# Performance work log

Hardware: AMD Instinct MI355X
Metric: run time of the kernel (lower is better)

## Reference

```python
import jax, jax.numpy as jnp
import numpy as np

B, S, D = 1, 2048, 4096
H, HK, HD = 32, 8, 128  # query heads, kv heads, head dim
T_CACHE = 2048
N_REP = H // HK


def setup_inputs() -> dict:
    key = jax.random.key(0)
    ks = jax.random.split(key, 8)
    x = jax.random.normal(ks[0], (B, S, D), dtype=jnp.float32)
    # multiplicative rope factor, broadcast over head axis
    rope = jax.random.uniform(ks[1], (1, S, 1, HD), dtype=jnp.float32, minval=-1.0, maxval=1.0)
    cache_k = jax.random.normal(ks[2], (B, T_CACHE, HK, HD), dtype=jnp.float32)
    cache_v = jax.random.normal(ks[3], (B, T_CACHE, HK, HD), dtype=jnp.float32)
    wq = jax.random.normal(ks[4], (D, H * HD), dtype=jnp.float32) * 0.02
    wk = jax.random.normal(ks[5], (D, HK * HD), dtype=jnp.float32) * 0.02
    wv = jax.random.normal(ks[6], (D, HK * HD), dtype=jnp.float32) * 0.02
    wo = jax.random.normal(ks[7], (H * HD, D), dtype=jnp.float32) * 0.02
    # mask: [1, 1, S, T_CACHE + S]; attend freely to cache, causal within new chunk
    neg = np.float32(-1e9)
    causal = np.triu(np.full((S, S), neg, dtype=np.float32), k=1)
    mask = np.concatenate([np.zeros((S, T_CACHE), dtype=np.float32), causal], axis=1)
    mask = jnp.asarray(mask)[None, None, :, :]
    return {"x": x, "rope": rope, "mask": mask, "cache_k": cache_k,
            "cache_v": cache_v, "wq": wq, "wk": wk, "wv": wv, "wo": wo}


def reference(x, rope, mask, cache_k, cache_v, wq, wk, wv, wo):
    b, s, _ = x.shape
    scale = 1.0 / np.sqrt(HD).astype(np.float32)
    xq = (x @ wq).reshape(b, s, H, HD) * rope          # [b, s, H, hd]
    xk = (x @ wk).reshape(b, s, HK, HD) * rope         # [b, s, HK, hd]
    xv = (x @ wv).reshape(b, s, HK, HD)
    keys = jnp.concatenate([cache_k, xk], axis=1)      # [b, t, HK, hd]
    vals = jnp.concatenate([cache_v, xv], axis=1)
    keys = jnp.repeat(keys, N_REP, axis=2)             # GQA repeat -> [b, t, H, hd]
    vals = jnp.repeat(vals, N_REP, axis=2)
    scores = jnp.einsum('bshd,bthd->bhst', xq, keys) * scale
    scores = scores + mask
    probs = jax.nn.softmax(scores.astype(jnp.float32), axis=-1).astype(xq.dtype)
    out = jnp.einsum('bhst,bthd->bshd', probs, vals).reshape(b, s, H * HD)
    return out @ wo
```

## Files before the change

kernel.cpp:

```cpp
#include <hip/hip_runtime.h>

typedef unsigned short u16;
typedef unsigned int   u32;
typedef short  s16x8 __attribute__((ext_vector_type(8)));
typedef float  f32x4 __attribute__((ext_vector_type(4)));

__device__ __forceinline__ u16 f2bf(float f) {
    union { float f; u32 i; } x; x.f = f;
    u32 r = x.i + 0x7FFFu + ((x.i >> 16) & 1u);
    return (u16)(r >> 16);
}

__device__ __forceinline__ void gld16(const void* g, void* l) {
    __builtin_amdgcn_global_load_lds((const __attribute__((address_space(1))) void*)g,
                                     (__attribute__((address_space(3))) void*)l,
                                     16, 0, 0);
}

__global__ __launch_bounds__(256)
void cast_bf16(const float* __restrict__ in, u16* __restrict__ out, int n4) {
    int g = blockIdx.x * 256 + threadIdx.x;
    if (g >= n4) return;
    float4 v = ((const float4*)in)[g];
    ushort4 o; o.x = f2bf(v.x); o.y = f2bf(v.y); o.z = f2bf(v.z); o.w = f2bf(v.w);
    ((ushort4*)out)[g] = o;
}

__global__ __launch_bounds__(256)
void tconv(const float* __restrict__ B, u16* __restrict__ Bt, int K, int N) {
    __shared__ float T[32][33];
    int n0 = blockIdx.x * 32, k0 = blockIdx.y * 32;
    int t = threadIdx.x;
    int r = t >> 3, c4 = (t & 7) * 4;
    float4 v = *(const float4*)&B[(size_t)(k0 + r) * N + n0 + c4];
    T[r][c4 + 0] = v.x; T[r][c4 + 1] = v.y; T[r][c4 + 2] = v.z; T[r][c4 + 3] = v.w;
    __syncthreads();
    ushort4 o;
    o.x = f2bf(T[c4 + 0][r]); o.y = f2bf(T[c4 + 1][r]);
    o.z = f2bf(T[c4 + 2][r]); o.w = f2bf(T[c4 + 3][r]);
    *(ushort4*)&Bt[(size_t)(n0 + r) * K + k0 + c4] = o;
}

__global__ __launch_bounds__(256)
void kcache_conv(const float* __restrict__ ck, u16* __restrict__ Kc) {
    int g = blockIdx.x * 256 + threadIdx.x;
    int d = (g & 31) * 4, kh = (g >> 5) & 7, t = g >> 8;
    float4 v = *(const float4*)&ck[(size_t)t * 1024 + kh * 128 + d];
    ushort4 o; o.x = f2bf(v.x); o.y = f2bf(v.y); o.z = f2bf(v.z); o.w = f2bf(v.w);
    *(ushort4*)&Kc[(size_t)kh * 524288 + (size_t)t * 128 + d] = o;
}

__global__ __launch_bounds__(256)
void vcache_conv(const float* __restrict__ cv, u16* __restrict__ Vt) {
    __shared__ float T[32][33];
    int t0 = blockIdx.x * 32, d0 = blockIdx.y * 32, kh = blockIdx.z;
    int t = threadIdx.x;
    int r = t >> 3, c4 = (t & 7) * 4;
    float4 v = *(const float4*)&cv[(size_t)(t0 + r) * 1024 + kh * 128 + d0 + c4];
    T[r][c4 + 0] = v.x; T[r][c4 + 1] = v.y; T[r][c4 + 2] = v.z; T[r][c4 + 3] = v.w;
    __syncthreads();
    ushort4 o;
    o.x = f2bf(T[c4 + 0][r]); o.y = f2bf(T[c4 + 1][r]);
    o.z = f2bf(T[c4 + 2][r]); o.w = f2bf(T[c4 + 3][r]);
    *(ushort4*)&Vt[(size_t)(kh * 128 + d0 + r) * 4096 + t0 + c4] = o;
}

__device__ __forceinline__ void gemm_core(const u16* __restrict__ A,
                                          const u16* __restrict__ Bt,
                                          int K, int m0,
                                          u16* As, u16* Bs, f32x4 acc[4][4])
{
    const int tid = threadIdx.x;
    const int lane = tid & 63, w = tid >> 6;
    const int quad = lane >> 4, l15 = lane & 15;
    const int mw = (w >> 1) * 64, nw = (w & 1) * 64;
    const int lrow = tid >> 2;
    const int lcol = ((tid & 3) ^ (lrow & 3)) * 8;
    const int rsw = l15 & 3;

    for (int k0 = 0; k0 < K; k0 += 32) {
        __syncthreads();
        gld16(A  + (size_t)(m0 +      lrow) * K + k0 + lcol, &As[w * 512]);
        gld16(A  + (size_t)(m0 + 64 + lrow) * K + k0 + lcol, &As[2048 + w * 512]);
        gld16(Bt + (size_t)(           lrow) * K + k0 + lcol, &Bs[w * 512]);
        gld16(Bt + (size_t)(      64 + lrow) * K + k0 + lcol, &Bs[2048 + w * 512]);
        __syncthreads();
        s16x8 af[4], bf[4];
        #pragma unroll
        for (int i = 0; i < 4; ++i)
            af[i] = *(const s16x8*)&As[(mw + i * 16 + l15) * 32 + (quad ^ rsw) * 8];
        #pragma unroll
        for (int j = 0; j < 4; ++j)
            bf[j] = *(const s16x8*)&Bs[(nw + j * 16 + l15) * 32 + (quad ^ rsw) * 8];
        #pragma unroll
        for (int i = 0; i < 4; ++i)
            #pragma unroll
            for (int j = 0; j < 4; ++j)
                acc[i][j] = __builtin_amdgcn_mfma_f32_16x16x32_bf16(
                    af[i], bf[j], acc[i][j], 0, 0, 0);
    }
}

__global__ __launch_bounds__(256, 2)
void gemm_qkv(const u16* __restrict__ A, const u16* __restrict__ Wq,
              const u16* __restrict__ Wk, const u16* __restrict__ Wv,
              u16* __restrict__ Qw, u16* __restrict__ Kc, u16* __restrict__ Vt,
              const float* __restrict__ rope)
{
    __shared__ u16 As[128 * 32];
    __shared__ u16 Bs[128 * 32];
    const int m0 = blockIdx.y * 128, n0 = blockIdx.x * 128;

    const u16* Bt;
    if (n0 < 4096)       Bt = Wq + (size_t)n0 * 4096;
    else if (n0 < 5120)  Bt = Wk + (size_t)(n0 - 4096) * 4096;
    else                 Bt = Wv + (size_t)(n0 - 5120) * 4096;

    f32x4 acc[4][4];
    #pragma unroll
    for (int i = 0; i < 4; ++i)
        #pragma unroll
        for (int j = 0; j < 4; ++j) acc[i][j] = (f32x4)0.f;

    gemm_core(A, Bt, 4096, m0, As, Bs, acc);

    const int lane = threadIdx.x & 63, w = threadIdx.x >> 6;
    const int quad = lane >> 4, l15 = lane & 15;
    const int mw = (w >> 1) * 64, nw = (w & 1) * 64;

    #pragma unroll
    for (int i = 0; i < 4; ++i) {
        #pragma unroll
        for (int j = 0; j < 4; ++j) {
            int mm = m0 + mw + i * 16 + quad * 4;
            int nn = n0 + nw + j * 16 + l15;
            if (nn < 4096) {
                #pragma unroll
                for (int r = 0; r < 4; ++r)
                    Qw[(size_t)(mm + r) * 4096 + nn] =
                        f2bf(acc[i][j][r] * rope[(size_t)(mm + r) * 128 + (nn & 127)]
                             * 0.08838834764831845f);
            } else if (nn < 5120) {
                #pragma unroll
                for (int r = 0; r < 4; ++r)
                    Kc[(size_t)((nn - 4096) >> 7) * 524288
                       + (size_t)(2048 + mm + r) * 128 + (nn & 127)] =
                        f2bf(acc[i][j][r] * rope[(size_t)(mm + r) * 128 + (nn & 127)]);
            } else {
                ushort4 o;
                o.x = f2bf(acc[i][j][0]); o.y = f2bf(acc[i][j][1]);
                o.z = f2bf(acc[i][j][2]); o.w = f2bf(acc[i][j][3]);
                *(ushort4*)&Vt[(size_t)(nn - 5120) * 4096 + 2048 + mm] = o;
            }
        }
    }
}

__global__ __launch_bounds__(256, 2)
void gemm_wo(const u16* __restrict__ A, const u16* __restrict__ Bt,
             float* __restrict__ C)
{
    __shared__ u16 As[128 * 32];
    __shared__ u16 Bs[128 * 32];
    const int m0 = blockIdx.y * 128, n0 = blockIdx.x * 128;

    f32x4 acc[4][4];
    #pragma unroll
    for (int i = 0; i < 4; ++i)
        #pragma unroll
        for (int j = 0; j < 4; ++j) acc[i][j] = (f32x4)0.f;

    gemm_core(A, Bt + (size_t)n0 * 4096, 4096, m0, As, Bs, acc);

    const int lane = threadIdx.x & 63, w = threadIdx.x >> 6;
    const int quad = lane >> 4, l15 = lane & 15;
    const int mw = (w >> 1) * 64, nw = (w & 1) * 64;

    #pragma unroll
    for (int i = 0; i < 4; ++i)
        #pragma unroll
        for (int j = 0; j < 4; ++j) {
            int mm = m0 + mw + i * 16 + quad * 4;
            int nn = n0 + nw + j * 16 + l15;
            #pragma unroll
            for (int r = 0; r < 4; ++r)
                C[(size_t)(mm + r) * 4096 + nn] = acc[i][j][r];
        }
}

__global__ __launch_bounds__(256, 2)
void attn_mfma(const u16* __restrict__ Qw, const u16* __restrict__ Kc,
               const u16* __restrict__ Vt, u16* __restrict__ AO)
{
    __shared__ u16 Ks[64 * 128];
    __shared__ u16 Vs[128 * 64];
    __shared__ u16 Qs[64 * 136];
    __shared__ u16 Pb[64 * 72];
    __shared__ float Ls[2][64];

    const int tid = threadIdx.x;
    const int lane = tid & 63, w = tid >> 6;
    const int quad = lane >> 4, l15 = lane & 15;
    const int h = blockIdx.x, kh = h >> 2;
    const int q0 = blockIdx.y * 64;
    const int kw = w & 1, qw = w >> 1;
    const size_t kvb = (size_t)kh * 524288;

    #pragma unroll
    for (int i = 0; i < 4; ++i) {
        int g = tid + i * 256;
        int row = g >> 4, c8 = (g & 15) * 8;
        *(s16x8*)&Qs[row * 136 + c8] =
            *(const s16x8*)&Qw[(size_t)(q0 + row) * 4096 + h * 128 + c8];
    }

    f32x4 o[2][4];
    #pragma unroll
    for (int m = 0; m < 2; ++m)
        #pragma unroll
        for (int n = 0; n < 4; ++n) o[m][n] = (f32x4)0.f;
    float lacc[2] = {0.f, 0.f};

    const int krow = tid >> 4, kcol = ((tid & 15) ^ (krow & 15)) * 8;
    const int vrow = tid >> 3, vcol = ((tid & 7) ^ (vrow & 7)) * 8;
    const int ksw = l15, vsw = l15 & 7;

    const int kend = 2112 + q0;
    for (int t0 = 0; t0 < kend; t0 += 64) {
        __syncthreads();
        #pragma unroll
        for (int i = 0; i < 4; ++i)
            gld16(Kc + kvb + (size_t)(t0 + i * 16 + krow) * 128 + kcol,
                  &Ks[i * 2048 + w * 512]);
        #pragma unroll
        for (int i = 0; i < 4; ++i)
            gld16(Vt + kvb + (size_t)(i * 32 + vrow) * 4096 + t0 + vcol,
                  &Vs[i * 2048 + w * 512]);
        __syncthreads();

        f32x4 sc[2][2];
        sc[0][0] = (f32x4)0.f; sc[0][1] = (f32x4)0.f;
        sc[1][0] = (f32x4)0.f; sc[1][1] = (f32x4)0.f;
        #pragma unroll
        for (int ks = 0; ks < 4; ++ks) {
            int kc8 = (((ks * 4 + quad) ^ ksw) & 15) * 8;
            s16x8 kf0 = *(const s16x8*)&Ks[(kw * 32 +      l15) * 128 + kc8];
            s16x8 kf1 = *(const s16x8*)&Ks[(kw * 32 + 16 + l15) * 128 + kc8];
            s16x8 qf0 = *(const s16x8*)&Qs[(qw * 32 +      l15) * 136 + ks * 32 + quad * 8];
            s16x8 qf1 = *(const s16x8*)&Qs[(qw * 32 + 16 + l15) * 136 + ks * 32 + quad * 8];
            sc[0][0] = __builtin_amdgcn_mfma_f32_16x16x32_bf16(kf0, qf0, sc[0][0], 0, 0, 0);
            sc[0][1] = __builtin_amdgcn_mfma_f32_16x16x32_bf16(kf0, qf1, sc[0][1], 0, 0, 0);
            sc[1][0] = __builtin_amdgcn_mfma_f32_16x16x32_bf16(kf1, qf0, sc[1][0], 0, 0, 0);
            sc[1][1] = __builtin_amdgcn_mfma_f32_16x16x32_bf16(kf1, qf1, sc[1][1], 0, 0, 0);
        }

        const bool maskt = (t0 + 63 > 2048 + q0);
        #pragma unroll
        for (int m2 = 0; m2 < 2; ++m2) {
            #pragma unroll
            for (int n2 = 0; n2 < 2; ++n2) {
                float e0 = __expf(sc[m2][n2][0]);
                float e1 = __expf(sc[m2][n2][1]);
                float e2 = __expf(sc[m2][n2][2]);
                float e3 = __expf(sc[m2][n2][3]);
                if (maskt) {
                    int key = t0 + kw * 32 + m2 * 16 + quad * 4;
                    int qv  = q0 + qw * 32 + n2 * 16 + l15;
                    if (key + 0 >= 2048 && key + 0 - 2048 > qv) e0 = 0.f;
                    if (key + 1 >= 2048 && key + 1 - 2048 > qv) e1 = 0.f;
                    if (key + 2 >= 2048 && key + 2 - 2048 > qv) e2 = 0.f;
                    if (key + 3 >= 2048 && key + 3 - 2048 > qv) e3 = 0.f;
                }
                lacc[n2] += (e0 + e1) + (e2 + e3);
                uint2 pk;
                pk.x = (u32)f2bf(e0) | ((u32)f2bf(e1) << 16);
                pk.y = (u32)f2bf(e2) | ((u32)f2bf(e3) << 16);
                *(uint2*)&Pb[(qw * 32 + n2 * 16 + l15) * 72 + kw * 32 + m2 * 16 + quad * 4] = pk;
            }
        }
        __syncthreads();

        #pragma unroll
        for (int ks = 0; ks < 2; ++ks) {
            int vc8 = (((ks * 4 + quad) ^ vsw) & 7) * 8;
            s16x8 vf0 = *(const s16x8*)&Vs[(w * 32 +      l15) * 64 + vc8];
            s16x8 vf1 = *(const s16x8*)&Vs[(w * 32 + 16 + l15) * 64 + vc8];
            #pragma unroll
            for (int n = 0; n < 4; ++n) {
                s16x8 pf = *(const s16x8*)&Pb[(n * 16 + l15) * 72 + ks * 32 + quad * 8];
                o[0][n] = __builtin_amdgcn_mfma_f32_16x16x32_bf16(vf0, pf, o[0][n], 0, 0, 0);
                o[1][n] = __builtin_amdgcn_mfma_f32_16x16x32_bf16(vf1, pf, o[1][n], 0, 0, 0);
            }
        }
    }

    lacc[0] += __shfl_xor(lacc[0], 16); lacc[0] += __shfl_xor(lacc[0], 32);
    lacc[1] += __shfl_xor(lacc[1], 16); lacc[1] += __shfl_xor(lacc[1], 32);
    if (lane < 16) {
        Ls[kw][qw * 32 +      lane] = lacc[0];
        Ls[kw][qw * 32 + 16 + lane] = lacc[1];
    }
    __syncthreads();

    #pragma unroll
    for (int n = 0; n < 4; ++n) {
        int qq = n * 16 + l15;
        float inv = 1.f / (Ls[0][qq] + Ls[1][qq]);
        #pragma unroll
        for (int m = 0; m < 2; ++m) {
            ushort4 ov;
            ov.x = f2bf(o[m][n][0] * inv);
            ov.y = f2bf(o[m][n][1] * inv);
            ov.z = f2bf(o[m][n][2] * inv);
            ov.w = f2bf(o[m][n][3] * inv);
            *(ushort4*)&AO[(size_t)(q0 + qq) * 4096 + h * 128
                           + w * 32 + m * 16 + quad * 4] = ov;
        }
    }
}

extern "C" void kernel_launch(void* const* d_in, const int* in_sizes, int n_in,
                              void* d_out, int out_size, void* d_ws, size_t ws_size,
                              hipStream_t stream)
{
    const float* x      = (const float*)d_in[0];
    const float* rope   = (const float*)d_in[1];
    const float* cacheK = (const float*)d_in[3];
    const float* cacheV = (const float*)d_in[4];
    const float* wq     = (const float*)d_in[5];
    const float* wk     = (const float*)d_in[6];
    const float* wv     = (const float*)d_in[7];
    const float* wo     = (const float*)d_in[8];
    float* out = (float*)d_out;

    u16* xb = (u16*)d_ws;
    u16* W0 = xb + (size_t)8388608;
    u16* W1 = W0 + (size_t)16777216;
    u16* Qw = W1 + (size_t)4194304;
    u16* Kc = Qw + (size_t)8388608;
    u16* Vt = Kc + (size_t)4194304;
    u16* AO = Vt + (size_t)4194304;
    u16* Wv = AO;

    dim3 blk(256);
    cast_bf16<<<dim3(8192), blk, 0, stream>>>(x, xb, 2097152);
    tconv<<<dim3(128, 128), blk, 0, stream>>>(wq, W0, 4096, 4096);
    tconv<<<dim3(32, 128), blk, 0, stream>>>(wk, W1, 4096, 1024);
    tconv<<<dim3(32, 128), blk, 0, stream>>>(wv, Wv, 4096, 1024);
    gemm_qkv<<<dim3(48, 16), blk, 0, stream>>>(xb, W0, W1, Wv, Qw, Kc, Vt, rope);
    kcache_conv<<<dim3(2048), blk, 0, stream>>>(cacheK, Kc);
    vcache_conv<<<dim3(64, 4, 8), blk, 0, stream>>>(cacheV, Vt);
    attn_mfma<<<dim3(32, 32), blk, 0, stream>>>(Qw, Kc, Vt, AO);
    tconv<<<dim3(128, 128), blk, 0, stream>>>(wo, W0, 4096, 4096);
    gemm_wo<<<dim3(32, 16), blk, 0, stream>>>(AO, W0, out);
}
```

Measured before the change: 612.9 us.

## Double-buffer K/V tiles in attention and keep Q fragments in registers

The attention kernel now uses two LDS buffers each for K and V. The next 64-key tile is prefetched with global_load_lds while the current tile's QK and PV MFMAs run. Q fragments are loaded once into registers instead of being staged through shared memory. The mid-loop barrier waits only on LDS counters, so outstanding global prefetches are not drained there. The cost is higher LDS use (about 73KB per block) and more VGPRs, which could limit occupancy at two blocks per CU.

```diff
diff --git a/kernel.cpp b/kernel.cpp
--- a/kernel.cpp
+++ b/kernel.cpp
@@ -192,9 +192,8 @@
 void attn_mfma(const u16* __restrict__ Qw, const u16* __restrict__ Kc,
                const u16* __restrict__ Vt, u16* __restrict__ AO)
 {
-    __shared__ u16 Ks[64 * 128];
-    __shared__ u16 Vs[128 * 64];
-    __shared__ u16 Qs[64 * 136];
+    __shared__ u16 Ks[2][64 * 128];
+    __shared__ u16 Vs[2][128 * 64];
     __shared__ u16 Pb[64 * 72];
     __shared__ float Ls[2][64];
 
@@ -206,13 +205,13 @@
     const int kw = w & 1, qw = w >> 1;
     const size_t kvb = (size_t)kh * 524288;
 
-    #pragma unroll
-    for (int i = 0; i < 4; ++i) {
-        int g = tid + i * 256;
-        int row = g >> 4, c8 = (g & 15) * 8;
-        *(s16x8*)&Qs[row * 136 + c8] =
-            *(const s16x8*)&Qw[(size_t)(q0 + row) * 4096 + h * 128 + c8];
-    }
+    s16x8 qreg[2][4];
+    #pragma unroll
+    for (int n = 0; n < 2; ++n)
+        #pragma unroll
+        for (int ks = 0; ks < 4; ++ks)
+            qreg[n][ks] = *(const s16x8*)&Qw[(size_t)(q0 + qw * 32 + n * 16 + l15) * 4096
+                                             + h * 128 + ks * 32 + quad * 8];
 
     f32x4 o[2][4];
     #pragma unroll
@@ -225,18 +224,33 @@
     const int vrow = tid >> 3, vcol = ((tid & 7) ^ (vrow & 7)) * 8;
     const int ksw = l15, vsw = l15 & 7;
 
+    const u16* kpg = Kc + kvb + (size_t)krow * 128 + kcol;
+    const u16* vpg = Vt + kvb + (size_t)vrow * 4096 + vcol;
+
     const int kend = 2112 + q0;
-    for (int t0 = 0; t0 < kend; t0 += 64) {
+
+    #pragma unroll
+    for (int i = 0; i < 4; ++i)
+        gld16(kpg + i * 2048, &Ks[0][i * 2048 + w * 512]);
+    #pragma unroll
+    for (int i = 0; i < 4; ++i)
+        gld16(vpg + (size_t)i * 131072, &Vs[0][i * 2048 + w * 512]);
+
+    int cur = 0;
+    for (int t0 = 0; t0 < kend; t0 += 64, cur ^= 1) {
         __syncthreads();
-        #pragma unroll
-        for (int i = 0; i < 4; ++i)
-            gld16(Kc + kvb + (size_t)(t0 + i * 16 + krow) * 128 + kcol,
-                  &Ks[i * 2048 + w * 512]);
-        #pragma unroll
-        for (int i = 0; i < 4; ++i)
-            gld16(Vt + kvb + (size_t)(i * 32 + vrow) * 4096 + t0 + vcol,
-                  &Vs[i * 2048 + w * 512]);
-        __syncthreads();
+
+        const int t1 = t0 + 64;
+        if (t1 < kend) {
+            #pragma unroll
+            for (int i = 0; i < 4; ++i)
+                gld16(kpg + (size_t)t1 * 128 + i * 2048,
+                      &Ks[cur ^ 1][i * 2048 + w * 512]);
+            #pragma unroll
+            for (int i = 0; i < 4; ++i)
+                gld16(vpg + (size_t)i * 131072 + t1,
+                      &Vs[cur ^ 1][i * 2048 + w * 512]);
+        }
 
         f32x4 sc[2][2];
         sc[0][0] = (f32x4)0.f; sc[0][1] = (f32x4)0.f;
@@ -244,14 +258,12 @@
         #pragma unroll
         for (int ks = 0; ks < 4; ++ks) {
             int kc8 = (((ks * 4 + quad) ^ ksw) & 15) * 8;
-            s16x8 kf0 = *(const s16x8*)&Ks[(kw * 32 +      l15) * 128 + kc8];
-            s16x8 kf1 = *(const s16x8*)&Ks[(kw * 32 + 16 + l15) * 128 + kc8];
-            s16x8 qf0 = *(const s16x8*)&Qs[(qw * 32 +      l15) * 136 + ks * 32 + quad * 8];
-            s16x8 qf1 = *(const s16x8*)&Qs[(qw * 32 + 16 + l15) * 136 + ks * 32 + quad * 8];
-            sc[0][0] = __builtin_amdgcn_mfma_f32_16x16x32_bf16(kf0, qf0, sc[0][0], 0, 0, 0);
-            sc[0][1] = __builtin_amdgcn_mfma_f32_16x16x32_bf16(kf0, qf1, sc[0][1], 0, 0, 0);
-            sc[1][0] = __builtin_amdgcn_mfma_f32_16x16x32_bf16(kf1, qf0, sc[1][0], 0, 0, 0);
-            sc[1][1] = __builtin_amdgcn_mfma_f32_16x16x32_bf16(kf1, qf1, sc[1][1], 0, 0, 0);
+            s16x8 kf0 = *(const s16x8*)&Ks[cur][(kw * 32 +      l15) * 128 + kc8];
+            s16x8 kf1 = *(const s16x8*)&Ks[cur][(kw * 32 + 16 + l15) * 128 + kc8];
+            sc[0][0] = __builtin_amdgcn_mfma_f32_16x16x32_bf16(kf0, qreg[0][ks], sc[0][0], 0, 0, 0);
+            sc[0][1] = __builtin_amdgcn_mfma_f32_16x16x32_bf16(kf0, qreg[1][ks], sc[0][1], 0, 0, 0);
+            sc[1][0] = __builtin_amdgcn_mfma_f32_16x16x32_bf16(kf1, qreg[0][ks], sc[1][0], 0, 0, 0);
+            sc[1][1] = __builtin_amdgcn_mfma_f32_16x16x32_bf16(kf1, qreg[1][ks], sc[1][1], 0, 0, 0);
         }
 
         const bool maskt = (t0 + 63 > 2048 + q0);
@@ -278,13 +290,16 @@
                 *(uint2*)&Pb[(qw * 32 + n2 * 16 + l15) * 72 + kw * 32 + m2 * 16 + quad * 4] = pk;
             }
         }
-        __syncthreads();
+
+        asm volatile("s_waitcnt lgkmcnt(0)" ::: "memory");
+        __builtin_amdgcn_s_barrier();
+        asm volatile("" ::: "memory");
 
         #pragma unroll
         for (int ks = 0; ks < 2; ++ks) {
             int vc8 = (((ks * 4 + quad) ^ vsw) & 7) * 8;
-            s16x8 vf0 = *(const s16x8*)&Vs[(w * 32 +      l15) * 64 + vc8];
-            s16x8 vf1 = *(const s16x8*)&Vs[(w * 32 + 16 + l15) * 64 + vc8];
+            s16x8 vf0 = *(const s16x8*)&Vs[cur][(w * 32 +      l15) * 64 + vc8];
+            s16x8 vf1 = *(const s16x8*)&Vs[cur][(w * 32 + 16 + l15) * 64 + vc8];
             #pragma unroll
             for (int n = 0; n < 4; ++n) {
                 s16x8 pf = *(const s16x8*)&Pb[(n * 16 + l15) * 72 + ks * 32 + quad * 8];
```

Result: no change. 607.3 us (-0.9%).
